# Kernel tuning notes

Measured on AMD Instinct MI355X. Metric: run time of the kernel, lower is better.

## Reference

```python
import jax, jax.numpy as jnp
import numpy as np

B, N, C = 4, 1024, 768
H, K, TEMP = 12, 32, 1.0
D = C // H
EPS = 1e-9


def setup_inputs() -> dict:
    key = jax.random.key(0)
    ks = jax.random.split(key, 5)
    x = jax.random.normal(ks[0], (B, N, C), dtype=jnp.float32)
    u = jax.random.uniform(ks[1], (B, N, N), dtype=jnp.float32)
    qkv_w = jax.random.normal(ks[2], (C, 3 * C), dtype=jnp.float32) * 0.02
    qkv_b = jnp.zeros((3 * C,), dtype=jnp.float32)
    proj_w = jax.random.normal(ks[3], (C, C), dtype=jnp.float32) * 0.02
    proj_b = jnp.zeros((C,), dtype=jnp.float32)
    head_scores = jnp.ones((H,), dtype=jnp.float32)
    return {"x": x, "u": u, "qkv_w": qkv_w, "qkv_b": qkv_b,
            "proj_w": proj_w, "proj_b": proj_b, "head_scores": head_scores}


def reference(x, u, qkv_w, qkv_b, proj_w, proj_b, head_scores):
    # qkv projection: [B,N,3C] -> [3,B,H,N,D]
    qkv = (x @ qkv_w + qkv_b).reshape(B, N, 3, H, D)
    qkv = jnp.transpose(qkv, (2, 0, 3, 1, 4))
    q, k, v = qkv[0], qkv[1], qkv[2]

    scale = 1.0 / np.sqrt(D)
    # full dense scores [B,H,N,N] (torch computes this twice; same math once)
    scores = jnp.einsum('bhnd,bhmd->bhnm', q, k) * scale

    # Gumbel top-K gate over head-averaged logits
    logits = scores.mean(axis=1)                         # [B,N,N]
    gumbel = -jnp.log(-jnp.log(u + EPS) + EPS)
    probs = jax.nn.softmax((logits + gumbel) / TEMP, axis=-1)
    topk_vals = jax.lax.top_k(probs, K)[0]               # sorted descending
    thresh = topk_vals[..., -1:]                          # K-th largest
    sparse_mask = (probs >= thresh).astype(scores.dtype)  # [B,N,N]

    # post-softmax masking (breaks flash fusion)
    attn = jax.nn.softmax(scores, axis=-1) * sparse_mask[:, None]
    out = jnp.einsum('bhnm,bhmd->bhnd', attn, v)          # [B,H,N,D]
    out = jnp.transpose(out, (0, 2, 1, 3)).reshape(B, N, C)
    return (out * head_scores.mean()) @ proj_w + proj_b
```

## Files before the change

### kernel.cpp

```cpp
#include <hip/hip_runtime.h>
#include <hip/hip_bf16.h>
#include <math.h>

#define B_ 4
#define N_ 1024
#define C_ 768
#define H_ 12
#define D_ 64
#define TOPK_ 32
#define EPS_ 1e-9f

#define LDN_ 32
#define LK_  72
#define QKS_ 1536

typedef __attribute__((ext_vector_type(8))) short bf16x8;
typedef __attribute__((ext_vector_type(4))) float f32x4;
typedef unsigned short u16;

struct TopkRec { unsigned int cnt; unsigned short c[62]; };

__device__ __forceinline__ u16 f2bf(float f) {
    unsigned int u = __float_as_uint(f);
    u += 0x7fffu + ((u >> 16) & 1u);
    return (u16)(u >> 16);
}
__device__ __forceinline__ float bf2f(u16 h) {
    return __uint_as_float(((unsigned int)h) << 16);
}

__device__ __forceinline__ void gll16(const void* g, void* l) {
    __builtin_amdgcn_global_load_lds(
        (const __attribute__((address_space(1))) void*)g,
        (__attribute__((address_space(3))) void*)l, 16, 0, 0);
}

__global__ __launch_bounds__(256) void conv_x(
    const float* __restrict__ X, u16* __restrict__ Xh, u16* __restrict__ Xl)
{
    const size_t off = ((size_t)blockIdx.x * 256 + threadIdx.x) * 8;
    float4 a = *(const float4*)&X[off];
    float4 b = *(const float4*)&X[off + 4];
    float v[8] = {a.x, a.y, a.z, a.w, b.x, b.y, b.z, b.w};
    u16 hb[8], lb[8];
    #pragma unroll
    for (int i = 0; i < 8; ++i) {
        u16 hi = f2bf(v[i]);
        hb[i] = hi;
        lb[i] = f2bf(v[i] - bf2f(hi));
    }
    *(bf16x8*)&Xh[off] = *(const bf16x8*)&hb[0];
    *(bf16x8*)&Xl[off] = *(const bf16x8*)&lb[0];
}

__global__ __launch_bounds__(256) void conv_w_nt(
    const float* __restrict__ W, u16* __restrict__ Wt_h, u16* __restrict__ Wt_l,
    int Kdim, int Ncols)
{
    __shared__ float Ts[64][65];
    const int t  = threadIdx.x;
    const int r  = t >> 2;
    const int cq = (t & 3) * 16;
    const int n0 = blockIdx.x * 64, k0 = blockIdx.y * 64;

    #pragma unroll
    for (int q = 0; q < 4; ++q) {
        float4 v = *(const float4*)&W[(size_t)(k0 + r) * Ncols + n0 + cq + q * 4];
        Ts[r][cq + q * 4 + 0] = v.x;
        Ts[r][cq + q * 4 + 1] = v.y;
        Ts[r][cq + q * 4 + 2] = v.z;
        Ts[r][cq + q * 4 + 3] = v.w;
    }
    __syncthreads();
    u16 hb[16], lb[16];
    #pragma unroll
    for (int i = 0; i < 16; ++i) {
        float val = Ts[cq + i][r];
        u16 hi = f2bf(val);
        hb[i] = hi;
        lb[i] = f2bf(val - bf2f(hi));
    }
    const size_t obase = (size_t)(n0 + r) * Kdim + k0 + cq;
    *(bf16x8*)&Wt_h[obase]     = *(const bf16x8*)&hb[0];
    *(bf16x8*)&Wt_h[obase + 8] = *(const bf16x8*)&hb[8];
    *(bf16x8*)&Wt_l[obase]     = *(const bf16x8*)&lb[0];
    *(bf16x8*)&Wt_l[obase + 8] = *(const bf16x8*)&lb[8];
}

__global__ __launch_bounds__(256) void gemm_qkv(
    const u16* __restrict__ Ath, const u16* __restrict__ Atl,
    const u16* __restrict__ Bth, const u16* __restrict__ Btl,
    const float* __restrict__ bias,
    u16* __restrict__ Ch, u16* __restrict__ Cl, float* __restrict__ Vf)
{
    __shared__ __align__(16) char smem[34816];
    u16* Ah = (u16*)(smem);
    u16* Al = (u16*)(smem + 8192);
    u16* Bh = (u16*)(smem + 16384);
    u16* Bl = (u16*)(smem + 24576);

    const int t    = threadIdx.x;
    const int d    = blockIdx.x;
    const int xcd  = d & 7, j = d >> 3;
    const int xt   = (xcd & 1) * 9 + (j % 9);
    const int yt   = (xcd >> 1) * 8 + (j / 9);
    const int m0   = yt * 128, n0 = xt * 128;
    const int lane = t & 63, w = t >> 6;
    const int wm   = (w >> 1) * 64, wn = (w & 1) * 64;
    const int fr   = lane & 15, kg8 = lane >> 4;
    const int w16  = w * 16;
    const int r4s  = lane >> 2, q4s = (lane & 3) * 8;

    f32x4 acc[4][4];
    #pragma unroll
    for (int i = 0; i < 4; ++i)
        #pragma unroll
        for (int j2 = 0; j2 < 4; ++j2)
            acc[i][j2] = (f32x4){0.f, 0.f, 0.f, 0.f};

    for (int kt = 0; kt < 24; ++kt) {
        const int k0 = kt * 32;
        __syncthreads();
        {
            const size_t ga0 = (size_t)(m0 + w16 + r4s) * C_ + k0 + q4s;
            const size_t ga1 = ga0 + (size_t)64 * C_;
            const size_t gb0 = (size_t)(n0 + w16 + r4s) * C_ + k0 + q4s;
            const size_t gb1 = gb0 + (size_t)64 * C_;
            gll16(&Ath[ga0], &Ah[w16 * LDN_]);
            gll16(&Ath[ga1], &Ah[(64 + w16) * LDN_]);
            gll16(&Atl[ga0], &Al[w16 * LDN_]);
            gll16(&Atl[ga1], &Al[(64 + w16) * LDN_]);
            gll16(&Bth[gb0], &Bh[w16 * LDN_]);
            gll16(&Bth[gb1], &Bh[(64 + w16) * LDN_]);
            gll16(&Btl[gb0], &Bl[w16 * LDN_]);
            gll16(&Btl[gb1], &Bl[(64 + w16) * LDN_]);
        }
        __syncthreads();

        bf16x8 aF[4], bF[4], a2F[4], b2F[4];
        #pragma unroll
        for (int fm = 0; fm < 4; ++fm)
            aF[fm] = *(const bf16x8*)&Ah[(wm + fm * 16 + fr) * LDN_ + kg8 * 8];
        #pragma unroll
        for (int fn = 0; fn < 4; ++fn)
            bF[fn] = *(const bf16x8*)&Bh[(wn + fn * 16 + fr) * LDN_ + kg8 * 8];
        #pragma unroll
        for (int fm = 0; fm < 4; ++fm)
            #pragma unroll
            for (int fn = 0; fn < 4; ++fn)
                acc[fm][fn] = __builtin_amdgcn_mfma_f32_16x16x32_bf16(
                    aF[fm], bF[fn], acc[fm][fn], 0, 0, 0);
        #pragma unroll
        for (int fn = 0; fn < 4; ++fn)
            b2F[fn] = *(const bf16x8*)&Bl[(wn + fn * 16 + fr) * LDN_ + kg8 * 8];
        #pragma unroll
        for (int fm = 0; fm < 4; ++fm)
            #pragma unroll
            for (int fn = 0; fn < 4; ++fn)
                acc[fm][fn] = __builtin_amdgcn_mfma_f32_16x16x32_bf16(
                    aF[fm], b2F[fn], acc[fm][fn], 0, 0, 0);
        #pragma unroll
        for (int fm = 0; fm < 4; ++fm)
            a2F[fm] = *(const bf16x8*)&Al[(wm + fm * 16 + fr) * LDN_ + kg8 * 8];
        #pragma unroll
        for (int fm = 0; fm < 4; ++fm)
            #pragma unroll
            for (int fn = 0; fn < 4; ++fn)
                acc[fm][fn] = __builtin_amdgcn_mfma_f32_16x16x32_bf16(
                    a2F[fm], bF[fn], acc[fm][fn], 0, 0, 0);
    }
    __syncthreads();

    const bool isV = (n0 >= 1536);
    float* Ts = (float*)(smem + w * 8448);
    const int lr8 = lane >> 3, lc8 = (lane & 7) * 8;
    #pragma unroll
    for (int p = 0; p < 2; ++p) {
        #pragma unroll
        for (int fmh = 0; fmh < 2; ++fmh) {
            const int fm = p * 2 + fmh;
            #pragma unroll
            for (int fn = 0; fn < 4; ++fn) {
                const float bv = bias[n0 + wn + fn * 16 + fr];
                #pragma unroll
                for (int i = 0; i < 4; ++i)
                    Ts[(fmh * 16 + kg8 * 4 + i) * 66 + fn * 16 + fr] =
                        acc[fm][fn][i] + bv;
            }
        }
        #pragma unroll
        for (int it = 0; it < 4; ++it) {
            const int r = it * 8 + lr8;
            float v[8];
            #pragma unroll
            for (int c = 0; c < 8; ++c) v[c] = Ts[r * 66 + lc8 + c];
            const int grow = m0 + wm + p * 32 + r;
            const int gcol = n0 + wn + lc8;
            if (isV) {
                float4 v0 = {v[0], v[1], v[2], v[3]};
                float4 v1 = {v[4], v[5], v[6], v[7]};
                float* vp = &Vf[(size_t)grow * C_ + gcol - 1536];
                *(float4*)vp       = v0;
                *(float4*)(vp + 4) = v1;
            } else {
                u16 hb[8], lb[8];
                #pragma unroll
                for (int c = 0; c < 8; ++c) {
                    u16 hi = f2bf(v[c]);
                    hb[c] = hi;
                    lb[c] = f2bf(v[c] - bf2f(hi));
                }
                *(bf16x8*)&Ch[(size_t)grow * QKS_ + gcol] = *(const bf16x8*)&hb[0];
                *(bf16x8*)&Cl[(size_t)grow * QKS_ + gcol] = *(const bf16x8*)&lb[0];
            }
        }
    }
}

__global__ __launch_bounds__(256) void attn_fused(
    const u16* __restrict__ qh, const u16* __restrict__ ql,
    const float* __restrict__ u, float* __restrict__ z,
    float2* __restrict__ mlp)
{
    __shared__ u16 KsH[128 * LK_], KsL[128 * LK_];

    const int t    = threadIdx.x;
    const int lane = t & 63, w = t >> 6;
    const int fr   = lane & 15, kg8 = lane >> 4;
    const int n0   = blockIdx.x * 64;
    const int m0   = blockIdx.y * 128;
    const int mc   = blockIdx.y;
    const int b    = blockIdx.z;

    f32x4 zacc[8];
    #pragma unroll
    for (int fn = 0; fn < 8; ++fn) zacc[fn] = (f32x4){0.f, 0.f, 0.f, 0.f};

    const int kr = t >> 1, kd = (t & 1) * 32;

    for (int hd = 0; hd < H_; ++hd) {
        const size_t qb = (size_t)(b * N_ + n0 + w * 16 + fr) * QKS_ + hd * 64 + kg8 * 8;
        bf16x8 aH0 = *(const bf16x8*)&qh[qb];
        bf16x8 aH1 = *(const bf16x8*)&qh[qb + 32];
        bf16x8 aL0 = *(const bf16x8*)&ql[qb];
        bf16x8 aL1 = *(const bf16x8*)&ql[qb + 32];

        const size_t kb = (size_t)(b * N_ + m0 + kr) * QKS_ + 768 + hd * 64 + kd;
        bf16x8 h0 = *(const bf16x8*)&qh[kb];
        bf16x8 h1 = *(const bf16x8*)&qh[kb + 8];
        bf16x8 h2 = *(const bf16x8*)&qh[kb + 16];
        bf16x8 h3 = *(const bf16x8*)&qh[kb + 24];
        bf16x8 l0 = *(const bf16x8*)&ql[kb];
        bf16x8 l1 = *(const bf16x8*)&ql[kb + 8];
        bf16x8 l2 = *(const bf16x8*)&ql[kb + 16];
        bf16x8 l3 = *(const bf16x8*)&ql[kb + 24];

        __syncthreads();
        const int sb = kr * LK_ + kd;
        *(bf16x8*)&KsH[sb]      = h0;  *(bf16x8*)&KsH[sb + 8]  = h1;
        *(bf16x8*)&KsH[sb + 16] = h2;  *(bf16x8*)&KsH[sb + 24] = h3;
        *(bf16x8*)&KsL[sb]      = l0;  *(bf16x8*)&KsL[sb + 8]  = l1;
        *(bf16x8*)&KsL[sb + 16] = l2;  *(bf16x8*)&KsL[sb + 24] = l3;
        __syncthreads();

        f32x4 acc[8];
        #pragma unroll
        for (int fn = 0; fn < 8; ++fn) acc[fn] = (f32x4){0.f, 0.f, 0.f, 0.f};

        #pragma unroll
        for (int fn = 0; fn < 8; ++fn) {
            const int bidx = (fn * 16 + fr) * LK_ + kg8 * 8;
            bf16x8 bH = *(const bf16x8*)&KsH[bidx];
            bf16x8 bL = *(const bf16x8*)&KsL[bidx];
            acc[fn] = __builtin_amdgcn_mfma_f32_16x16x32_bf16(aH0, bH, acc[fn], 0, 0, 0);
            acc[fn] = __builtin_amdgcn_mfma_f32_16x16x32_bf16(aH0, bL, acc[fn], 0, 0, 0);
            acc[fn] = __builtin_amdgcn_mfma_f32_16x16x32_bf16(aL0, bH, acc[fn], 0, 0, 0);
        }
        #pragma unroll
        for (int fn = 0; fn < 8; ++fn) {
            const int bidx = (fn * 16 + fr) * LK_ + 32 + kg8 * 8;
            bf16x8 bH = *(const bf16x8*)&KsH[bidx];
            bf16x8 bL = *(const bf16x8*)&KsL[bidx];
            acc[fn] = __builtin_amdgcn_mfma_f32_16x16x32_bf16(aH1, bH, acc[fn], 0, 0, 0);
            acc[fn] = __builtin_amdgcn_mfma_f32_16x16x32_bf16(aH1, bL, acc[fn], 0, 0, 0);
            acc[fn] = __builtin_amdgcn_mfma_f32_16x16x32_bf16(aL1, bH, acc[fn], 0, 0, 0);
        }

        #pragma unroll
        for (int fn = 0; fn < 8; ++fn) {
            zacc[fn][0] += acc[fn][0];
            zacc[fn][1] += acc[fn][1];
            zacc[fn][2] += acc[fn][2];
            zacc[fn][3] += acc[fn][3];
        }

        #pragma unroll
        for (int reg = 0; reg < 4; ++reg) {
            float tmax = acc[0][reg];
            #pragma unroll
            for (int fn = 1; fn < 8; ++fn) tmax = fmaxf(tmax, acc[fn][reg]);
            tmax *= 0.125f;
            tmax = fmaxf(tmax, __shfl_xor(tmax, 1));
            tmax = fmaxf(tmax, __shfl_xor(tmax, 2));
            tmax = fmaxf(tmax, __shfl_xor(tmax, 4));
            tmax = fmaxf(tmax, __shfl_xor(tmax, 8));
            float tsum = 0.f;
            #pragma unroll
            for (int fn = 0; fn < 8; ++fn)
                tsum += expf(acc[fn][reg] * 0.125f - tmax);
            tsum += __shfl_xor(tsum, 1);
            tsum += __shfl_xor(tsum, 2);
            tsum += __shfl_xor(tsum, 4);
            tsum += __shfl_xor(tsum, 8);
            if (fr == 0) {
                const int n = n0 + w * 16 + kg8 * 4 + reg;
                mlp[(((size_t)(b * H_ + hd)) * N_ + n) * 8 + mc] =
                    make_float2(tmax, tsum);
            }
        }
    }

    const float sc = 0.125f / 12.0f;
    #pragma unroll
    for (int fn = 0; fn < 8; ++fn) {
        const int m = m0 + fn * 16 + fr;
        #pragma unroll
        for (int reg = 0; reg < 4; ++reg) {
            const int n = n0 + w * 16 + kg8 * 4 + reg;
            const float uv = u[((size_t)(b * N_ + n)) * N_ + m];
            const float g  = -logf(-logf(uv + EPS_) + EPS_);
            z[((size_t)(b * N_ + n)) * N_ + m] = zacc[fn][reg] * sc + g;
        }
    }
}

__global__ __launch_bounds__(256) void ml_merge(
    const float2* __restrict__ mlp, float2* __restrict__ ml)
{
    const size_t idx = (size_t)blockIdx.x * 256 + threadIdx.x;
    float2 p[8];
    #pragma unroll
    for (int i = 0; i < 8; ++i) p[i] = mlp[idx * 8 + i];
    float m = p[0].x;
    #pragma unroll
    for (int i = 1; i < 8; ++i) m = fmaxf(m, p[i].x);
    float l = 0.f;
    #pragma unroll
    for (int i = 0; i < 8; ++i) l += p[i].y * expf(p[i].x - m);
    ml[idx] = make_float2(m, l);
}

__global__ __launch_bounds__(64) void topk_cols_kernel(
    const float* __restrict__ z, TopkRec* __restrict__ recs)
{
    const int row  = blockIdx.x;
    const int lane = threadIdx.x;
    const float* zr = z + (size_t)row * N_;
    float zv[16], wk[16];
    #pragma unroll
    for (int j = 0; j < 16; ++j) { zv[j] = zr[lane + 64 * j]; wk[j] = zv[j]; }

    float thresh = -INFINITY;
    for (int it = 0; it < TOPK_; ++it) {
        float lm = wk[0]; int li = 0;
        #pragma unroll
        for (int j = 1; j < 16; ++j)
            if (wk[j] > lm) { lm = wk[j]; li = j; }
        float gm = lm;
        gm = fmaxf(gm, __shfl_xor(gm, 1));
        gm = fmaxf(gm, __shfl_xor(gm, 2));
        gm = fmaxf(gm, __shfl_xor(gm, 4));
        gm = fmaxf(gm, __shfl_xor(gm, 8));
        gm = fmaxf(gm, __shfl_xor(gm, 16));
        gm = fmaxf(gm, __shfl_xor(gm, 32));
        unsigned long long has = __ballot(lm == gm);
        int first = __ffsll((unsigned long long)has) - 1;
        if (lane == first) wk[li] = -INFINITY;
        thresh = gm;
    }

    const unsigned long long below = ((unsigned long long)1 << lane) - 1;
    unsigned int basec = 0;
    TopkRec* rec = recs + row;
    #pragma unroll
    for (int j = 0; j < 16; ++j) {
        unsigned long long wmask = __ballot(zv[j] >= thresh);
        if (zv[j] >= thresh) {
            unsigned int pos = basec + (unsigned int)__popcll(wmask & below);
            if (pos < 62u) rec->c[pos] = (unsigned short)(lane + 64 * j);
        }
        basec += (unsigned int)__popcll(wmask);
    }
    if (lane == 0) rec->cnt = basec > 62u ? 62u : basec;
}

__global__ __launch_bounds__(256) void sparse_pv_kernel(
    const u16* __restrict__ qh, const u16* __restrict__ ql,
    const float* __restrict__ Vf,
    const TopkRec* __restrict__ recs, const float2* __restrict__ ml,
    const float* __restrict__ head_scores,
    u16* __restrict__ out1h, u16* __restrict__ out1l)
{
    __shared__ int cols_s[62];
    __shared__ int cnt_s;

    const int t    = threadIdx.x;
    const int lane = t & 63, wv = t >> 6;
    const int c4   = lane >> 2;
    const int dq   = lane & 3;
    const int row  = blockIdx.x;
    const int b    = row >> 10, n = row & 1023;

    const TopkRec* rec = recs + row;
    if (t == 0) cnt_s = (int)min(rec->cnt, 62u);
    if (t < 62) cols_s[t] = rec->c[t];

    float hsum = 0.f;
    #pragma unroll
    for (int i = 0; i < H_; ++i) hsum += head_scores[i];
    const float hs_mean = hsum * (1.0f / 12.0f);
    __syncthreads();
    const int cnt = cnt_s;
    const int nbatch = (cnt + 15) >> 4;

    for (int hd = wv; hd < H_; hd += 4) {
        float qv[16];
        {
            const size_t qb = (size_t)row * QKS_ + hd * 64 + dq * 16;
            bf16x8 qh0 = *(const bf16x8*)&qh[qb], qh1 = *(const bf16x8*)&qh[qb + 8];
            bf16x8 ql0 = *(const bf16x8*)&ql[qb], ql1 = *(const bf16x8*)&ql[qb + 8];
            #pragma unroll
            for (int i = 0; i < 8; ++i) {
                qv[i]     = bf2f((u16)qh0[i]) + bf2f((u16)ql0[i]);
                qv[i + 8] = bf2f((u16)qh1[i]) + bf2f((u16)ql1[i]);
            }
        }
        const float2 mlv = ml[((size_t)(b * H_ + hd)) * N_ + n];

        float acc[16];
        #pragma unroll
        for (int i = 0; i < 16; ++i) acc[i] = 0.f;

        for (int batch = 0; batch < nbatch; ++batch) {
            const int cidx  = batch * 16 + c4;
            const bool valid = (cidx < cnt);
            const int col   = cols_s[valid ? cidx : cnt - 1];

            const size_t kb = (size_t)(b * N_ + col) * QKS_ + 768 + hd * 64 + dq * 16;
            bf16x8 kh0 = *(const bf16x8*)&qh[kb], kh1 = *(const bf16x8*)&qh[kb + 8];
            bf16x8 kl0 = *(const bf16x8*)&ql[kb], kl1 = *(const bf16x8*)&ql[kb + 8];
            float dot = 0.f;
            #pragma unroll
            for (int i = 0; i < 8; ++i) {
                dot += qv[i]     * (bf2f((u16)kh0[i]) + bf2f((u16)kl0[i]));
                dot += qv[i + 8] * (bf2f((u16)kh1[i]) + bf2f((u16)kl1[i]));
            }
            dot += __shfl_xor(dot, 1);
            dot += __shfl_xor(dot, 2);
            float p = valid ? expf(dot * 0.125f - mlv.x) : 0.f;

            const float* vb = &Vf[(size_t)(b * N_ + col) * C_ + hd * 64 + dq * 16];
            #pragma unroll
            for (int q = 0; q < 4; ++q) {
                float4 v4 = *(const float4*)&vb[q * 4];
                acc[q * 4 + 0] += p * v4.x;
                acc[q * 4 + 1] += p * v4.y;
                acc[q * 4 + 2] += p * v4.z;
                acc[q * 4 + 3] += p * v4.w;
            }
        }

        #pragma unroll
        for (int d = 4; d < 64; d <<= 1)
            #pragma unroll
            for (int i = 0; i < 16; ++i)
                acc[i] += __shfl_xor(acc[i], d);

        if (c4 == 0) {
            const float s = hs_mean / mlv.y;
            u16 hb[16], lb[16];
            #pragma unroll
            for (int i = 0; i < 16; ++i) {
                float val = acc[i] * s;
                u16 hi = f2bf(val);
                hb[i] = hi;
                lb[i] = f2bf(val - bf2f(hi));
            }
            const size_t ob = (size_t)row * C_ + hd * 64 + dq * 16;
            *(bf16x8*)&out1h[ob]     = *(const bf16x8*)&hb[0];
            *(bf16x8*)&out1h[ob + 8] = *(const bf16x8*)&hb[8];
            *(bf16x8*)&out1l[ob]     = *(const bf16x8*)&lb[0];
            *(bf16x8*)&out1l[ob + 8] = *(const bf16x8*)&lb[8];
        }
    }
}

__global__ __launch_bounds__(256) void gemm_proj(
    const u16* __restrict__ Ath, const u16* __restrict__ Atl,
    const u16* __restrict__ Bth, const u16* __restrict__ Btl,
    const float* __restrict__ bias, float* __restrict__ Cm)
{
    __shared__ __align__(16) char smem[34816];
    u16* Ah = (u16*)(smem);
    u16* Al = (u16*)(smem + 8192);
    u16* Bh = (u16*)(smem + 16384);
    u16* Bl = (u16*)(smem + 24576);

    const int t    = threadIdx.x;
    const int d    = blockIdx.x;
    const int xcd  = d & 7, j = d >> 3;
    const int xt   = j % 6;
    const int yt   = xcd * 4 + (j / 6);
    const int m0   = yt * 128, n0 = xt * 128;
    const int lane = t & 63, w = t >> 6;
    const int wm   = (w >> 1) * 64, wn = (w & 1) * 64;
    const int fr   = lane & 15, kg8 = lane >> 4;
    const int w16  = w * 16;
    const int r4s  = lane >> 2, q4s = (lane & 3) * 8;

    f32x4 acc[4][4];
    #pragma unroll
    for (int i = 0; i < 4; ++i)
        #pragma unroll
        for (int j2 = 0; j2 < 4; ++j2)
            acc[i][j2] = (f32x4){0.f, 0.f, 0.f, 0.f};

    for (int kt = 0; kt < 24; ++kt) {
        const int k0 = kt * 32;
        __syncthreads();
        {
            const size_t ga0 = (size_t)(m0 + w16 + r4s) * C_ + k0 + q4s;
            const size_t ga1 = ga0 + (size_t)64 * C_;
            const size_t gb0 = (size_t)(n0 + w16 + r4s) * C_ + k0 + q4s;
            const size_t gb1 = gb0 + (size_t)64 * C_;
            gll16(&Ath[ga0], &Ah[w16 * LDN_]);
            gll16(&Ath[ga1], &Ah[(64 + w16) * LDN_]);
            gll16(&Atl[ga0], &Al[w16 * LDN_]);
            gll16(&Atl[ga1], &Al[(64 + w16) * LDN_]);
            gll16(&Bth[gb0], &Bh[w16 * LDN_]);
            gll16(&Bth[gb1], &Bh[(64 + w16) * LDN_]);
            gll16(&Btl[gb0], &Bl[w16 * LDN_]);
            gll16(&Btl[gb1], &Bl[(64 + w16) * LDN_]);
        }
        __syncthreads();

        bf16x8 aF[4], bF[4], a2F[4], b2F[4];
        #pragma unroll
        for (int fm = 0; fm < 4; ++fm)
            aF[fm] = *(const bf16x8*)&Ah[(wm + fm * 16 + fr) * LDN_ + kg8 * 8];
        #pragma unroll
        for (int fn = 0; fn < 4; ++fn)
            bF[fn] = *(const bf16x8*)&Bh[(wn + fn * 16 + fr) * LDN_ + kg8 * 8];
        #pragma unroll
        for (int fm = 0; fm < 4; ++fm)
            #pragma unroll
            for (int fn = 0; fn < 4; ++fn)
                acc[fm][fn] = __builtin_amdgcn_mfma_f32_16x16x32_bf16(
                    aF[fm], bF[fn], acc[fm][fn], 0, 0, 0);
        #pragma unroll
        for (int fn = 0; fn < 4; ++fn)
            b2F[fn] = *(const bf16x8*)&Bl[(wn + fn * 16 + fr) * LDN_ + kg8 * 8];
        #pragma unroll
        for (int fm = 0; fm < 4; ++fm)
            #pragma unroll
            for (int fn = 0; fn < 4; ++fn)
                acc[fm][fn] = __builtin_amdgcn_mfma_f32_16x16x32_bf16(
                    aF[fm], b2F[fn], acc[fm][fn], 0, 0, 0);
        #pragma unroll
        for (int fm = 0; fm < 4; ++fm)
            a2F[fm] = *(const bf16x8*)&Al[(wm + fm * 16 + fr) * LDN_ + kg8 * 8];
        #pragma unroll
        for (int fm = 0; fm < 4; ++fm)
            #pragma unroll
            for (int fn = 0; fn < 4; ++fn)
                acc[fm][fn] = __builtin_amdgcn_mfma_f32_16x16x32_bf16(
                    a2F[fm], bF[fn], acc[fm][fn], 0, 0, 0);
    }
    __syncthreads();

    float* Ts = (float*)(smem + w * 8448);
    const int lr8 = lane >> 3, lc8 = (lane & 7) * 8;
    #pragma unroll
    for (int p = 0; p < 2; ++p) {
        #pragma unroll
        for (int fmh = 0; fmh < 2; ++fmh) {
            const int fm = p * 2 + fmh;
            #pragma unroll
            for (int fn = 0; fn < 4; ++fn) {
                const float bv = bias[n0 + wn + fn * 16 + fr];
                #pragma unroll
                for (int i = 0; i < 4; ++i)
                    Ts[(fmh * 16 + kg8 * 4 + i) * 66 + fn * 16 + fr] =
                        acc[fm][fn][i] + bv;
            }
        }
        #pragma unroll
        for (int it = 0; it < 4; ++it) {
            const int r = it * 8 + lr8;
            float v[8];
            #pragma unroll
            for (int c = 0; c < 8; ++c) v[c] = Ts[r * 66 + lc8 + c];
            const int grow = m0 + wm + p * 32 + r;
            const int gcol = n0 + wn + lc8;
            float4 v0 = {v[0], v[1], v[2], v[3]};
            float4 v1 = {v[4], v[5], v[6], v[7]};
            float* cp = &Cm[(size_t)grow * C_ + gcol];
            *(float4*)cp       = v0;
            *(float4*)(cp + 4) = v1;
        }
    }
}

extern "C" void kernel_launch(void* const* d_in, const int* in_sizes, int n_in,
                              void* d_out, int out_size, void* d_ws, size_t ws_size,
                              hipStream_t stream)
{
    (void)in_sizes; (void)n_in; (void)out_size; (void)ws_size;
    const float* x           = (const float*)d_in[0];
    const float* u           = (const float*)d_in[1];
    const float* qkv_w       = (const float*)d_in[2];
    const float* qkv_b       = (const float*)d_in[3];
    const float* proj_w      = (const float*)d_in[4];
    const float* proj_b      = (const float*)d_in[5];
    const float* head_scores = (const float*)d_in[6];
    float* out = (float*)d_out;

    char* ws = (char*)d_ws;
    u16*     qkv_h  = (u16*)ws;
    u16*     qkv_l  = (u16*)(ws + 12582912);
    float*   Vf     = (float*)(ws + 25165824);
    char*    R      = ws + 37748736;
    u16*     wq_t_h = (u16*)R;
    u16*     wq_t_l = (u16*)(R + 3538944);
    float*   z      = (float*)R;
    TopkRec* recs   = (TopkRec*)(R + 16777216);
    u16*     wp_t_h = (u16*)R;
    u16*     wp_t_l = (u16*)(R + 1179648);
    float2*  ml     = (float2*)(R + 2359296);
    u16*     out1h  = (u16*)(R + 2752512);
    u16*     out1l  = (u16*)(R + 9043968);
    u16*     x_h    = (u16*)d_out;
    u16*     x_l    = (u16*)((char*)d_out + 6291456);
    float2*  mlp    = (float2*)d_out;

    conv_x<<<dim3(4096 * 768 / 8 / 256), dim3(256), 0, stream>>>(x, x_h, x_l);

    conv_w_nt<<<dim3(2304 / 64, 768 / 64), dim3(256), 0, stream>>>(
        qkv_w, wq_t_h, wq_t_l, 768, 2304);

    gemm_qkv<<<dim3(576), dim3(256), 0, stream>>>(
        x_h, x_l, wq_t_h, wq_t_l, qkv_b, qkv_h, qkv_l, Vf);

    attn_fused<<<dim3(16, 8, B_), dim3(256), 0, stream>>>(
        qkv_h, qkv_l, u, z, mlp);

    topk_cols_kernel<<<dim3(B_ * N_), dim3(64), 0, stream>>>(z, recs);

    conv_w_nt<<<dim3(768 / 64, 768 / 64), dim3(256), 0, stream>>>(
        proj_w, wp_t_h, wp_t_l, 768, 768);

    ml_merge<<<dim3(B_ * H_ * N_ / 256), dim3(256), 0, stream>>>(mlp, ml);

    sparse_pv_kernel<<<dim3(B_ * N_), dim3(256), 0, stream>>>(
        qkv_h, qkv_l, Vf, recs, ml, head_scores, out1h, out1l);

    gemm_proj<<<dim3(192), dim3(256), 0, stream>>>(
        out1h, out1l, wp_t_h, wp_t_l, proj_b, out);
}
```

Before: 280.1 us.

## Prefetch next head's Q/K in attention loop and halve projection GEMM tile height

The attention score kernel now double-buffers Q and K register loads across heads. It issues the global loads for the next head before computing the current one, so memory latency overlaps with the MFMA work. The projection GEMM switches from 128x128 to 64x128 tiles and launches 384 blocks instead of 192, giving more blocks across the CUs. In exchange the attention kernel holds more live registers, which can lower occupancy, and the smaller GEMM tile reuses each loaded operand less.

```diff
diff --git a/kernel.cpp b/kernel.cpp
--- a/kernel.cpp
+++ b/kernel.cpp
@@ -236,56 +236,57 @@
     #pragma unroll
     for (int fn = 0; fn < 8; ++fn) zacc[fn] = (f32x4){0.f, 0.f, 0.f, 0.f};
 
-    const int kr = t >> 1, kd = (t & 1) * 32;
-
-    for (int hd = 0; hd < H_; ++hd) {
+    const int skr = t >> 1, skd = (t & 1) * 32;
+
+    bf16x8 kAr[8], kBr[8], qAr[4], qBr[4];
+
+    auto loadK = [&](bf16x8 (&kr)[8], int hd) {
+        const size_t kb = (size_t)(b * N_ + m0 + skr) * QKS_ + 768 + hd * 64 + skd;
+        kr[0] = *(const bf16x8*)&qh[kb];
+        kr[1] = *(const bf16x8*)&qh[kb + 8];
+        kr[2] = *(const bf16x8*)&qh[kb + 16];
+        kr[3] = *(const bf16x8*)&qh[kb + 24];
+        kr[4] = *(const bf16x8*)&ql[kb];
+        kr[5] = *(const bf16x8*)&ql[kb + 8];
+        kr[6] = *(const bf16x8*)&ql[kb + 16];
+        kr[7] = *(const bf16x8*)&ql[kb + 24];
+    };
+    auto loadQ = [&](bf16x8 (&qr)[4], int hd) {
         const size_t qb = (size_t)(b * N_ + n0 + w * 16 + fr) * QKS_ + hd * 64 + kg8 * 8;
-        bf16x8 aH0 = *(const bf16x8*)&qh[qb];
-        bf16x8 aH1 = *(const bf16x8*)&qh[qb + 32];
-        bf16x8 aL0 = *(const bf16x8*)&ql[qb];
-        bf16x8 aL1 = *(const bf16x8*)&ql[qb + 32];
-
-        const size_t kb = (size_t)(b * N_ + m0 + kr) * QKS_ + 768 + hd * 64 + kd;
-        bf16x8 h0 = *(const bf16x8*)&qh[kb];
-        bf16x8 h1 = *(const bf16x8*)&qh[kb + 8];
-        bf16x8 h2 = *(const bf16x8*)&qh[kb + 16];
-        bf16x8 h3 = *(const bf16x8*)&qh[kb + 24];
-        bf16x8 l0 = *(const bf16x8*)&ql[kb];
-        bf16x8 l1 = *(const bf16x8*)&ql[kb + 8];
-        bf16x8 l2 = *(const bf16x8*)&ql[kb + 16];
-        bf16x8 l3 = *(const bf16x8*)&ql[kb + 24];
-
-        __syncthreads();
-        const int sb = kr * LK_ + kd;
-        *(bf16x8*)&KsH[sb]      = h0;  *(bf16x8*)&KsH[sb + 8]  = h1;
-        *(bf16x8*)&KsH[sb + 16] = h2;  *(bf16x8*)&KsH[sb + 24] = h3;
-        *(bf16x8*)&KsL[sb]      = l0;  *(bf16x8*)&KsL[sb + 8]  = l1;
-        *(bf16x8*)&KsL[sb + 16] = l2;  *(bf16x8*)&KsL[sb + 24] = l3;
-        __syncthreads();
-
+        qr[0] = *(const bf16x8*)&qh[qb];
+        qr[1] = *(const bf16x8*)&qh[qb + 32];
+        qr[2] = *(const bf16x8*)&ql[qb];
+        qr[3] = *(const bf16x8*)&ql[qb + 32];
+    };
+    auto writeK = [&](const bf16x8 (&kr)[8]) {
+        const int sb = skr * LK_ + skd;
+        *(bf16x8*)&KsH[sb]      = kr[0];  *(bf16x8*)&KsH[sb + 8]  = kr[1];
+        *(bf16x8*)&KsH[sb + 16] = kr[2];  *(bf16x8*)&KsH[sb + 24] = kr[3];
+        *(bf16x8*)&KsL[sb]      = kr[4];  *(bf16x8*)&KsL[sb + 8]  = kr[5];
+        *(bf16x8*)&KsL[sb + 16] = kr[6];  *(bf16x8*)&KsL[sb + 24] = kr[7];
+    };
+    auto compute = [&](const bf16x8 (&qr)[4], int hd) {
         f32x4 acc[8];
         #pragma unroll
         for (int fn = 0; fn < 8; ++fn) acc[fn] = (f32x4){0.f, 0.f, 0.f, 0.f};
-
         #pragma unroll
         for (int fn = 0; fn < 8; ++fn) {
             const int bidx = (fn * 16 + fr) * LK_ + kg8 * 8;
             bf16x8 bH = *(const bf16x8*)&KsH[bidx];
             bf16x8 bL = *(const bf16x8*)&KsL[bidx];
-            acc[fn] = __builtin_amdgcn_mfma_f32_16x16x32_bf16(aH0, bH, acc[fn], 0, 0, 0);
-            acc[fn] = __builtin_amdgcn_mfma_f32_16x16x32_bf16(aH0, bL, acc[fn], 0, 0, 0);
-            acc[fn] = __builtin_amdgcn_mfma_f32_16x16x32_bf16(aL0, bH, acc[fn], 0, 0, 0);
+            acc[fn] = __builtin_amdgcn_mfma_f32_16x16x32_bf16(qr[0], bH, acc[fn], 0, 0, 0);
+            acc[fn] = __builtin_amdgcn_mfma_f32_16x16x32_bf16(qr[0], bL, acc[fn], 0, 0, 0);
+            acc[fn] = __builtin_amdgcn_mfma_f32_16x16x32_bf16(qr[2], bH, acc[fn], 0, 0, 0);
         }
         #pragma unroll
         for (int fn = 0; fn < 8; ++fn) {
             const int bidx = (fn * 16 + fr) * LK_ + 32 + kg8 * 8;
             bf16x8 bH = *(const bf16x8*)&KsH[bidx];
             bf16x8 bL = *(const bf16x8*)&KsL[bidx];
-            acc[fn] = __builtin_amdgcn_mfma_f32_16x16x32_bf16(aH1, bH, acc[fn], 0, 0, 0);
-            acc[fn] = __builtin_amdgcn_mfma_f32_16x16x32_bf16(aH1, bL, acc[fn], 0, 0, 0);
-            acc[fn] = __builtin_amdgcn_mfma_f32_16x16x32_bf16(aL1, bH, acc[fn], 0, 0, 0);
-        }
-
+            acc[fn] = __builtin_amdgcn_mfma_f32_16x16x32_bf16(qr[1], bH, acc[fn], 0, 0, 0);
+            acc[fn] = __builtin_amdgcn_mfma_f32_16x16x32_bf16(qr[1], bL, acc[fn], 0, 0, 0);
+            acc[fn] = __builtin_amdgcn_mfma_f32_16x16x32_bf16(qr[3], bH, acc[fn], 0, 0, 0);
+        }
         #pragma unroll
         for (int fn = 0; fn < 8; ++fn) {
             zacc[fn][0] += acc[fn][0];
@@ -293,7 +294,6 @@
             zacc[fn][2] += acc[fn][2];
             zacc[fn][3] += acc[fn][3];
         }
-
         #pragma unroll
         for (int reg = 0; reg < 4; ++reg) {
             float tmax = acc[0][reg];
@@ -318,6 +318,26 @@
                     make_float2(tmax, tsum);
             }
         }
+    };
+
+    loadQ(qAr, 0);
+    loadK(kAr, 0);
+    for (int hp = 0; hp < 6; ++hp) {
+        const int hd0 = hp * 2, hd1 = hp * 2 + 1;
+        __syncthreads();
+        writeK(kAr);
+        __syncthreads();
+        loadQ(qBr, hd1);
+        loadK(kBr, hd1);
+        compute(qAr, hd0);
+        __syncthreads();
+        writeK(kBr);
+        __syncthreads();
+        if (hp < 5) {
+            loadQ(qAr, hd0 + 2);
+            loadK(kAr, hd0 + 2);
+        }
+        compute(qBr, hd1);
     }
 
     const float sc = 0.125f / 12.0f;
@@ -500,27 +520,27 @@
     const u16* __restrict__ Bth, const u16* __restrict__ Btl,
     const float* __restrict__ bias, float* __restrict__ Cm)
 {
-    __shared__ __align__(16) char smem[34816];
+    __shared__ __align__(16) char smem[33792];
     u16* Ah = (u16*)(smem);
-    u16* Al = (u16*)(smem + 8192);
-    u16* Bh = (u16*)(smem + 16384);
-    u16* Bl = (u16*)(smem + 24576);
+    u16* Al = (u16*)(smem + 4096);
+    u16* Bh = (u16*)(smem + 8192);
+    u16* Bl = (u16*)(smem + 16384);
 
     const int t    = threadIdx.x;
     const int d    = blockIdx.x;
     const int xcd  = d & 7, j = d >> 3;
     const int xt   = j % 6;
-    const int yt   = xcd * 4 + (j / 6);
-    const int m0   = yt * 128, n0 = xt * 128;
+    const int yt   = xcd * 8 + j / 6;
+    const int m0   = yt * 64, n0 = xt * 128;
     const int lane = t & 63, w = t >> 6;
-    const int wm   = (w >> 1) * 64, wn = (w & 1) * 64;
+    const int wm   = (w & 1) * 32, wn = (w >> 1) * 64;
     const int fr   = lane & 15, kg8 = lane >> 4;
     const int w16  = w * 16;
     const int r4s  = lane >> 2, q4s = (lane & 3) * 8;
 
-    f32x4 acc[4][4];
-    #pragma unroll
-    for (int i = 0; i < 4; ++i)
+    f32x4 acc[2][4];
+    #pragma unroll
+    for (int i = 0; i < 2; ++i)
         #pragma unroll
         for (int j2 = 0; j2 < 4; ++j2)
             acc[i][j2] = (f32x4){0.f, 0.f, 0.f, 0.f};
@@ -529,30 +549,27 @@
         const int k0 = kt * 32;
         __syncthreads();
         {
-            const size_t ga0 = (size_t)(m0 + w16 + r4s) * C_ + k0 + q4s;
-            const size_t ga1 = ga0 + (size_t)64 * C_;
-            const size_t gb0 = (size_t)(n0 + w16 + r4s) * C_ + k0 + q4s;
-            const size_t gb1 = gb0 + (size_t)64 * C_;
-            gll16(&Ath[ga0], &Ah[w16 * LDN_]);
-            gll16(&Ath[ga1], &Ah[(64 + w16) * LDN_]);
-            gll16(&Atl[ga0], &Al[w16 * LDN_]);
-            gll16(&Atl[ga1], &Al[(64 + w16) * LDN_]);
-            gll16(&Bth[gb0], &Bh[w16 * LDN_]);
-            gll16(&Bth[gb1], &Bh[(64 + w16) * LDN_]);
-            gll16(&Btl[gb0], &Bl[w16 * LDN_]);
-            gll16(&Btl[gb1], &Bl[(64 + w16) * LDN_]);
-        }
-        __syncthreads();
-
-        bf16x8 aF[4], bF[4], a2F[4], b2F[4];
-        #pragma unroll
-        for (int fm = 0; fm < 4; ++fm)
+            const size_t ga  = (size_t)(m0 + w16 + r4s) * C_ + k0 + q4s;
+            const size_t gb0 = (size_t)(n0 + w * 32 + r4s) * C_ + k0 + q4s;
+            const size_t gb1 = gb0 + (size_t)16 * C_;
+            gll16(&Ath[ga],  &Ah[w16 * LDN_]);
+            gll16(&Atl[ga],  &Al[w16 * LDN_]);
+            gll16(&Bth[gb0], &Bh[(w * 32) * LDN_]);
+            gll16(&Bth[gb1], &Bh[(w * 32 + 16) * LDN_]);
+            gll16(&Btl[gb0], &Bl[(w * 32) * LDN_]);
+            gll16(&Btl[gb1], &Bl[(w * 32 + 16) * LDN_]);
+        }
+        __syncthreads();
+
+        bf16x8 aF[2], bF[4], a2F[2], b2F[4];
+        #pragma unroll
+        for (int fm = 0; fm < 2; ++fm)
             aF[fm] = *(const bf16x8*)&Ah[(wm + fm * 16 + fr) * LDN_ + kg8 * 8];
         #pragma unroll
         for (int fn = 0; fn < 4; ++fn)
             bF[fn] = *(const bf16x8*)&Bh[(wn + fn * 16 + fr) * LDN_ + kg8 * 8];
         #pragma unroll
-        for (int fm = 0; fm < 4; ++fm)
+        for (int fm = 0; fm < 2; ++fm)
             #pragma unroll
             for (int fn = 0; fn < 4; ++fn)
                 acc[fm][fn] = __builtin_amdgcn_mfma_f32_16x16x32_bf16(
@@ -561,16 +578,16 @@
         for (int fn = 0; fn < 4; ++fn)
             b2F[fn] = *(const bf16x8*)&Bl[(wn + fn * 16 + fr) * LDN_ + kg8 * 8];
         #pragma unroll
-        for (int fm = 0; fm < 4; ++fm)
+        for (int fm = 0; fm < 2; ++fm)
             #pragma unroll
             for (int fn = 0; fn < 4; ++fn)
                 acc[fm][fn] = __builtin_amdgcn_mfma_f32_16x16x32_bf16(
                     aF[fm], b2F[fn], acc[fm][fn], 0, 0, 0);
         #pragma unroll
-        for (int fm = 0; fm < 4; ++fm)
+        for (int fm = 0; fm < 2; ++fm)
             a2F[fm] = *(const bf16x8*)&Al[(wm + fm * 16 + fr) * LDN_ + kg8 * 8];
         #pragma unroll
-        for (int fm = 0; fm < 4; ++fm)
+        for (int fm = 0; fm < 2; ++fm)
             #pragma unroll
             for (int fn = 0; fn < 4; ++fn)
                 acc[fm][fn] = __builtin_amdgcn_mfma_f32_16x16x32_bf16(
@@ -581,33 +598,28 @@
     float* Ts = (float*)(smem + w * 8448);
     const int lr8 = lane >> 3, lc8 = (lane & 7) * 8;
     #pragma unroll
-    for (int p = 0; p < 2; ++p) {
-        #pragma unroll
-        for (int fmh = 0; fmh < 2; ++fmh) {
-            const int fm = p * 2 + fmh;
-            #pragma unroll
-            for (int fn = 0; fn < 4; ++fn) {
-                const float bv = bias[n0 + wn + fn * 16 + fr];
-                #pragma unroll
-                for (int i = 0; i < 4; ++i)
-                    Ts[(fmh * 16 + kg8 * 4 + i) * 66 + fn * 16 + fr] =
-                        acc[fm][fn][i] + bv;
-            }
-        }
-        #pragma unroll
-        for (int it = 0; it < 4; ++it) {
-            const int r = it * 8 + lr8;
-            float v[8];
-            #pragma unroll
-            for (int c = 0; c < 8; ++c) v[c] = Ts[r * 66 + lc8 + c];
-            const int grow = m0 + wm + p * 32 + r;
-            const int gcol = n0 + wn + lc8;
-            float4 v0 = {v[0], v[1], v[2], v[3]};
-            float4 v1 = {v[4], v[5], v[6], v[7]};
-            float* cp = &Cm[(size_t)grow * C_ + gcol];
-            *(float4*)cp       = v0;
-            *(float4*)(cp + 4) = v1;
-        }
+    for (int fm = 0; fm < 2; ++fm)
+        #pragma unroll
+        for (int fn = 0; fn < 4; ++fn) {
+            const float bv = bias[n0 + wn + fn * 16 + fr];
+            #pragma unroll
+            for (int i = 0; i < 4; ++i)
+                Ts[(fm * 16 + kg8 * 4 + i) * 66 + fn * 16 + fr] =
+                    acc[fm][fn][i] + bv;
+        }
+    #pragma unroll
+    for (int it = 0; it < 4; ++it) {
+        const int r = it * 8 + lr8;
+        float v[8];
+        #pragma unroll
+        for (int c = 0; c < 8; ++c) v[c] = Ts[r * 66 + lc8 + c];
+        const int grow = m0 + wm + r;
+        const int gcol = n0 + wn + lc8;
+        float4 v0 = {v[0], v[1], v[2], v[3]};
+        float4 v1 = {v[4], v[5], v[6], v[7]};
+        float* cp = &Cm[(size_t)grow * C_ + gcol];
+        *(float4*)cp       = v0;
+        *(float4*)(cp + 4) = v1;
     }
 }
 
@@ -664,6 +676,6 @@
     sparse_pv_kernel<<<dim3(B_ * N_), dim3(256), 0, stream>>>(
         qkv_h, qkv_l, Vf, recs, ml, head_scores, out1h, out1l);
 
-    gemm_proj<<<dim3(192), dim3(256), 0, stream>>>(
+    gemm_proj<<<dim3(384), dim3(256), 0, stream>>>(
         out1h, out1l, wp_t_h, wp_t_l, proj_b, out);
 }
```

Measured after the change: 269.5 us. 1.04x faster.
